# Optimization experiments

Measured on AMD Instinct MI355X. Metric: run time of the kernel, lower is better.

The kernel has to match this reference:

```python
import jax, jax.numpy as jnp
import numpy as np

PUPIL = 256          # pupil / OPD grid size
OUTPUT_DIM = 64      # cropped PSF postage-stamp size
N_BINS = 8           # number of SED wavelength bins
BATCH = 16
# Static, wavelength-dependent diffraction padding sizes (phase_N per bin).
# In the original these come from packed_SED_data[:,0,:] but are constant in a FoV.
PHASE_NS = [1024, 988, 952, 918, 886, 856, 828, 802]


def setup_inputs() -> dict:
    key = jax.random.key(0)
    k1, k2, k3 = jax.random.split(key, 3)
    # OPD in meters: small wavefront errors (~lambda/10 rms)
    opd_batch = jax.random.normal(k1, (BATCH, PUPIL, PUPIL), dtype=jnp.float32) * 1e-7
    # Annular pupil: outer aperture with central obscuration (like Euclid/VIS optics)
    yy, xx = np.mgrid[:PUPIL, :PUPIL].astype(np.float32)
    c = (PUPIL - 1) / 2.0
    r = np.sqrt((xx - c) ** 2 + (yy - c) ** 2) / (PUPIL / 2.0)
    obscurations = jnp.asarray(((r <= 1.0) & (r >= 0.3)).astype(np.float32))
    # Observed wavelengths per bin, in meters (visible band)
    lambdas = jnp.linspace(0.55e-6, 0.9e-6, N_BINS).astype(jnp.float32)
    # Normalized SED weights
    sed = jax.random.uniform(k2, (N_BINS,), dtype=jnp.float32) + 0.1
    sed_norms = sed / jnp.sum(sed)
    return {
        "opd_batch": opd_batch,
        "obscurations": obscurations,
        "lambdas": lambdas,
        "sed_norms": sed_norms,
    }


def _mono_psf(opd, obsc, lam, phase_N, out_dim):
    """Batched monochromatic PSF: OPD -> phase -> padded FFT -> cropped |.|^2, unit-sum."""
    # opd: [B, p, p]; phase = exp(i * 2pi/lambda * opd) * obscurations
    pre_phase = (2.0 * jnp.pi / lam) * opd
    phase = (jnp.cos(pre_phase) + 1j * jnp.sin(pre_phase)).astype(jnp.complex64)
    phase = phase * obsc.astype(jnp.complex64)
    p = opd.shape[-1]
    pad_lo = (phase_N - p) // 2
    pad_hi = phase_N - p - pad_lo
    padded = jnp.pad(phase, ((0, 0), (pad_lo, pad_hi), (pad_lo, pad_hi)))  # [B, N, N]
    fft = jnp.fft.fftshift(jnp.fft.fft2(padded), axes=(-2, -1))
    psf = fft.real ** 2 + fft.imag ** 2  # |FFT|^2, float32
    start = phase_N // 2 - out_dim // 2
    psf = psf[:, start:start + out_dim, start:start + out_dim]  # central crop
    return psf / jnp.sum(psf, axis=(-2, -1), keepdims=True)


def reference(opd_batch, obscurations, lambdas, sed_norms):
    # Polychromatic PSF: SED-weighted sum of monochromatic PSFs over wavelength bins.
    # Loop is over the small fixed set of bins (distinct static FFT sizes);
    # each bin is fully vectorized over the batch.
    out = jnp.zeros((opd_batch.shape[0], OUTPUT_DIM, OUTPUT_DIM), dtype=jnp.float32)
    for b, phase_N in enumerate(PHASE_NS):
        out = out + sed_norms[b] * _mono_psf(
            opd_batch, obscurations, lambdas[b], phase_N, OUTPUT_DIM
        )
    return out
```

## Files before the change

kernel.cpp:

```cpp
#include <hip/hip_runtime.h>
#include <math.h>

#define PUPIL 256
#define N_BINS 8
#define BATCH 16

__constant__ int PHASE_NS_C[N_BINS] = {1024, 988, 952, 918, 886, 856, 828, 802};

typedef short bf16x8 __attribute__((ext_vector_type(8)));
typedef float f32x4  __attribute__((ext_vector_type(4)));
typedef int   i32x4  __attribute__((ext_vector_type(4)));

#define MFMA16(a, b, c) __builtin_amdgcn_mfma_f32_16x16x32_bf16((a), (b), (c), 0, 0, 0)

__device__ __forceinline__ short f2bf(float f) {
  unsigned u = __float_as_uint(f);
  u += 0x7FFFu + ((u >> 16) & 1u);
  return (short)(u >> 16);
}
__device__ __forceinline__ bf16x8 neg8(bf16x8 v) {
  i32x4 t = __builtin_bit_cast(i32x4, v);
  t ^= (int)0x80008000;
  return __builtin_bit_cast(bf16x8, t);
}


__global__ void wprep(short* __restrict__ Wr_t, short* __restrict__ Wi_t) {
  int idx = blockIdx.x * 256 + threadIdx.x;
  int n   = idx & 255;
  int k   = (idx >> 8) & 63;
  int bin = idx >> 14;
  int N = PHASE_NS_C[bin];
  int m = ((k - 32) * n) % N;
  if (m < 0) m += N;
  float ang = -6.283185307179586f * (float)m / (float)N;
  float s, c;
  sincosf(ang, &s, &c);
  Wr_t[idx] = f2bf(c);
  Wi_t[idx] = f2bf(s);
}

__global__ __launch_bounds__(256, 1) void fused(
    const float* __restrict__ opd, const float* __restrict__ obsc,
    const float* __restrict__ lambdas,
    const short* __restrict__ Wr_t, const short* __restrict__ Wi_t,
    float* __restrict__ psf_raw, float* __restrict__ sums)
{
  const int tid = threadIdx.x;
  const int khalf = blockIdx.x, bin = blockIdx.y, b = blockIdx.z;
  const int bb = b * N_BINS + bin;
  const float w0 = 6.283185307179586f / lambdas[bin];

  __shared__ short Pr[256 * 40], Pi[256 * 40];
  __shared__ short Gr[32 * 264], Gi[32 * 264];
  __shared__ float pvbuf[64 * 33];
  __shared__ float red[4];

  const int wave = tid >> 6, lane = tid & 63;
  const int lr = lane & 15, lq = lane >> 4;

  f32x4 aR[2][4], aI[2][4];
  #pragma unroll
  for (int m = 0; m < 2; ++m)
    #pragma unroll
    for (int t = 0; t < 4; ++t) { aR[m][t] = (f32x4)0.0f; aI[m][t] = (f32x4)0.0f; }

  const int gy0 = tid >> 2;
  const int gx  = (tid & 3) * 8;
  const short* wr0 = Wr_t + ((size_t)bin * 64 + khalf * 32 + lr) * 256 + lq * 8;
  const short* wi0 = Wi_t + ((size_t)bin * 64 + khalf * 32 + lr) * 256 + lq * 8;

  for (int xc = 0; xc < 8; ++xc) {
    const int xb = xc * 32;
    bf16x8 vr[4], vi[4];
    #pragma unroll
    for (int i = 0; i < 4; ++i) {
      const int y = gy0 + i * 64;
      const float* orow = opd + ((size_t)b * PUPIL + y) * PUPIL + xb + gx;
      const float* brow = obsc + (size_t)y * PUPIL + xb + gx;
      float od[8], ob[8];
      *(float4*)&od[0] = *(const float4*)orow;
      *(float4*)&od[4] = *(const float4*)(orow + 4);
      *(float4*)&ob[0] = *(const float4*)brow;
      *(float4*)&ob[4] = *(const float4*)(brow + 4);
      #pragma unroll
      for (int j = 0; j < 8; ++j) {
        float s, c;
        __sincosf(w0 * od[j], &s, &c);
        vr[i][j] = f2bf(c * ob[j]);
        vi[i][j] = f2bf(s * ob[j]);
      }
    }
    __syncthreads();
    #pragma unroll
    for (int i = 0; i < 4; ++i) {
      const int y = gy0 + i * 64;
      *(bf16x8*)&Pr[y * 40 + gx] = vr[i];
      *(bf16x8*)&Pi[y * 40 + gx] = vi[i];
    }
    const bf16x8 w_r0  = *(const bf16x8*)(wr0 + xb);
    const bf16x8 w_r1  = *(const bf16x8*)(wr0 + 16 * 256 + xb);
    const bf16x8 w_i0  = *(const bf16x8*)(wi0 + xb);
    const bf16x8 w_i1  = *(const bf16x8*)(wi0 + 16 * 256 + xb);
    const bf16x8 nw_i0 = neg8(w_i0);
    const bf16x8 nw_i1 = neg8(w_i1);
    __syncthreads();

    for (int t = 0; t < 4; ++t) {
      const int y = wave * 64 + t * 16 + lr;
      const bf16x8 pr = *(const bf16x8*)&Pr[y * 40 + lq * 8];
      const bf16x8 pi = *(const bf16x8*)&Pi[y * 40 + lq * 8];
      aR[0][t] = MFMA16(w_r0,  pr, aR[0][t]);
      aR[0][t] = MFMA16(nw_i0, pi, aR[0][t]);
      aI[0][t] = MFMA16(w_r0,  pi, aI[0][t]);
      aI[0][t] = MFMA16(w_i0,  pr, aI[0][t]);
      aR[1][t] = MFMA16(w_r1,  pr, aR[1][t]);
      aR[1][t] = MFMA16(nw_i1, pi, aR[1][t]);
      aI[1][t] = MFMA16(w_r1,  pi, aI[1][t]);
      aI[1][t] = MFMA16(w_i1,  pr, aI[1][t]);
    }
  }

  #pragma unroll
  for (int m = 0; m < 2; ++m)
    #pragma unroll
    for (int t = 0; t < 4; ++t) {
      const int y = wave * 64 + t * 16 + lr;
      #pragma unroll
      for (int r = 0; r < 4; ++r) {
        const int kvl = m * 16 + lq * 4 + r;
        Gr[kvl * 264 + y] = f2bf(aR[m][t][r]);
        Gi[kvl * 264 + y] = f2bf(aI[m][t][r]);
      }
    }
  __syncthreads();

  f32x4 hR[2], hI[2];
  hR[0] = (f32x4)0.0f; hR[1] = (f32x4)0.0f;
  hI[0] = (f32x4)0.0f; hI[1] = (f32x4)0.0f;

  for (int yc = 0; yc < 8; ++yc) {
    const int yb2 = yc * 32;
    const size_t wo = ((size_t)bin * 64 + wave * 16 + lr) * 256 + yb2 + lq * 8;
    const bf16x8 w_r = *(const bf16x8*)(Wr_t + wo);
    const bf16x8 w_i = *(const bf16x8*)(Wi_t + wo);
    #pragma unroll
    for (int m = 0; m < 2; ++m) {
      const bf16x8 g_r = *(const bf16x8*)&Gr[(m * 16 + lr) * 264 + yb2 + lq * 8];
      const bf16x8 g_i = *(const bf16x8*)&Gi[(m * 16 + lr) * 264 + yb2 + lq * 8];
      const bf16x8 ng_i = neg8(g_i);
      hR[m] = MFMA16(g_r,  w_r, hR[m]);
      hR[m] = MFMA16(ng_i, w_i, hR[m]);
      hI[m] = MFMA16(g_r,  w_i, hI[m]);
      hI[m] = MFMA16(g_i,  w_r, hI[m]);
    }
  }

  float pv[2][4];
  float lsum = 0.f;
  #pragma unroll
  for (int m = 0; m < 2; ++m)
    #pragma unroll
    for (int r = 0; r < 4; ++r) {
      pv[m][r] = hR[m][r] * hR[m][r] + hI[m][r] * hI[m][r];
      lsum += pv[m][r];
    }
  #pragma unroll
  for (int off = 32; off > 0; off >>= 1) lsum += __shfl_down(lsum, off);
  if (lane == 0) red[wave] = lsum;

  const int u = wave * 16 + lr;
  #pragma unroll
  for (int m = 0; m < 2; ++m)
    #pragma unroll
    for (int r = 0; r < 4; ++r)
      pvbuf[u * 33 + m * 16 + lq * 4 + r] = pv[m][r];
  __syncthreads();

  if (tid == 0)
    sums[bb * 2 + khalf] = red[0] + red[1] + red[2] + red[3];

  #pragma unroll
  for (int k2 = 0; k2 < 8; ++k2) {
    const int i = tid + k2 * 256;
    const int uu = i >> 5, vl = i & 31;
    psf_raw[(size_t)bb * 4096 + uu * 64 + khalf * 32 + vl] = pvbuf[uu * 33 + vl];
  }
}

__global__ void combine(const float* __restrict__ psf_raw,
                        const float* __restrict__ sums,
                        const float* __restrict__ sed,
                        float* __restrict__ out) {
  __shared__ float sc[N_BINS];
  const int blk = blockIdx.x;
  const int b = blk >> 4;
  const int px = (blk & 15) * 256 + threadIdx.x;
  if (threadIdx.x < N_BINS) {
    const int bb = b * N_BINS + threadIdx.x;
    sc[threadIdx.x] = sed[threadIdx.x] / (sums[bb * 2] + sums[bb * 2 + 1]);
  }
  __syncthreads();
  float acc = 0.f;
  #pragma unroll
  for (int bin = 0; bin < N_BINS; ++bin)
    acc += sc[bin] * psf_raw[(size_t)(b * N_BINS + bin) * 4096 + px];
  out[b * 4096 + px] = acc;
}

extern "C" void kernel_launch(void* const* d_in, const int* in_sizes, int n_in,
                              void* d_out, int out_size, void* d_ws, size_t ws_size,
                              hipStream_t stream) {
  const float* opd     = (const float*)d_in[0];
  const float* obsc    = (const float*)d_in[1];
  const float* lambdas = (const float*)d_in[2];
  const float* sed     = (const float*)d_in[3];
  float* out = (float*)d_out;

  short* Wr_t   = (short*)d_ws;
  short* Wi_t   = Wr_t + (size_t)N_BINS * 64 * 256;
  float* psf_raw = (float*)(Wi_t + (size_t)N_BINS * 64 * 256);
  float* sums    = psf_raw + (size_t)BATCH * N_BINS * 4096;

  wprep<<<512, 256, 0, stream>>>(Wr_t, Wi_t);
  fused<<<dim3(2, N_BINS, BATCH), 256, 0, stream>>>(opd, obsc, lambdas,
                                                    Wr_t, Wi_t, psf_raw, sums);
  combine<<<256, 256, 0, stream>>>(psf_raw, sums, sed, out);
}
```

Measured before the change: 84.18 us.

## Double block size to 512 threads and use fast twiddle computation

```diff
diff --git a/kernel.cpp b/kernel.cpp
--- a/kernel.cpp
+++ b/kernel.cpp
@@ -31,16 +31,15 @@
   int k   = (idx >> 8) & 63;
   int bin = idx >> 14;
   int N = PHASE_NS_C[bin];
-  int m = ((k - 32) * n) % N;
-  if (m < 0) m += N;
-  float ang = -6.283185307179586f * (float)m / (float)N;
+  float f = __fdividef((float)((k - 32) * n), (float)N);
+  float rev = f - floorf(f);
   float s, c;
-  sincosf(ang, &s, &c);
+  __sincosf(-6.283185307179586f * rev, &s, &c);
   Wr_t[idx] = f2bf(c);
   Wi_t[idx] = f2bf(s);
 }
 
-__global__ __launch_bounds__(256, 1) void fused(
+__global__ __launch_bounds__(512, 2) void fused(
     const float* __restrict__ opd, const float* __restrict__ obsc,
     const float* __restrict__ lambdas,
     const short* __restrict__ Wr_t, const short* __restrict__ Wi_t,
@@ -51,19 +50,22 @@
   const int bb = b * N_BINS + bin;
   const float w0 = 6.283185307179586f / lambdas[bin];
 
-  __shared__ short Pr[256 * 40], Pi[256 * 40];
-  __shared__ short Gr[32 * 264], Gi[32 * 264];
-  __shared__ float pvbuf[64 * 33];
-  __shared__ float red[4];
+  __shared__ __align__(16) char smem[20480 * 2 + 16896 * 2 + 32];
+  short* Pr    = (short*)smem;
+  short* Pi    = (short*)(smem + 20480);
+  short* Gr    = (short*)(smem + 40960);
+  short* Gi    = (short*)(smem + 57856);
+  float* red   = (float*)(smem + 74752);
+  float* pvbuf = (float*)smem;
 
   const int wave = tid >> 6, lane = tid & 63;
   const int lr = lane & 15, lq = lane >> 4;
 
-  f32x4 aR[2][4], aI[2][4];
+  f32x4 aR[2][2], aI[2][2];
   #pragma unroll
   for (int m = 0; m < 2; ++m)
     #pragma unroll
-    for (int t = 0; t < 4; ++t) { aR[m][t] = (f32x4)0.0f; aI[m][t] = (f32x4)0.0f; }
+    for (int t = 0; t < 2; ++t) { aR[m][t] = (f32x4)0.0f; aI[m][t] = (f32x4)0.0f; }
 
   const int gy0 = tid >> 2;
   const int gx  = (tid & 3) * 8;
@@ -72,10 +74,10 @@
 
   for (int xc = 0; xc < 8; ++xc) {
     const int xb = xc * 32;
-    bf16x8 vr[4], vi[4];
-    #pragma unroll
-    for (int i = 0; i < 4; ++i) {
-      const int y = gy0 + i * 64;
+    bf16x8 vr[2], vi[2];
+    #pragma unroll
+    for (int i = 0; i < 2; ++i) {
+      const int y = gy0 + i * 128;
       const float* orow = opd + ((size_t)b * PUPIL + y) * PUPIL + xb + gx;
       const float* brow = obsc + (size_t)y * PUPIL + xb + gx;
       float od[8], ob[8];
@@ -91,13 +93,6 @@
         vi[i][j] = f2bf(s * ob[j]);
       }
     }
-    __syncthreads();
-    #pragma unroll
-    for (int i = 0; i < 4; ++i) {
-      const int y = gy0 + i * 64;
-      *(bf16x8*)&Pr[y * 40 + gx] = vr[i];
-      *(bf16x8*)&Pi[y * 40 + gx] = vi[i];
-    }
     const bf16x8 w_r0  = *(const bf16x8*)(wr0 + xb);
     const bf16x8 w_r1  = *(const bf16x8*)(wr0 + 16 * 256 + xb);
     const bf16x8 w_i0  = *(const bf16x8*)(wi0 + xb);
@@ -105,9 +100,16 @@
     const bf16x8 nw_i0 = neg8(w_i0);
     const bf16x8 nw_i1 = neg8(w_i1);
     __syncthreads();
-
-    for (int t = 0; t < 4; ++t) {
-      const int y = wave * 64 + t * 16 + lr;
+    #pragma unroll
+    for (int i = 0; i < 2; ++i) {
+      const int y = gy0 + i * 128;
+      *(bf16x8*)&Pr[y * 40 + gx] = vr[i];
+      *(bf16x8*)&Pi[y * 40 + gx] = vi[i];
+    }
+    __syncthreads();
+
+    for (int t = 0; t < 2; ++t) {
+      const int y = wave * 32 + t * 16 + lr;
       const bf16x8 pr = *(const bf16x8*)&Pr[y * 40 + lq * 8];
       const bf16x8 pi = *(const bf16x8*)&Pi[y * 40 + lq * 8];
       aR[0][t] = MFMA16(w_r0,  pr, aR[0][t]);
@@ -124,8 +126,8 @@
   #pragma unroll
   for (int m = 0; m < 2; ++m)
     #pragma unroll
-    for (int t = 0; t < 4; ++t) {
-      const int y = wave * 64 + t * 16 + lr;
+    for (int t = 0; t < 2; ++t) {
+      const int y = wave * 32 + t * 16 + lr;
       #pragma unroll
       for (int r = 0; r < 4; ++r) {
         const int kvl = m * 16 + lq * 4 + r;
@@ -135,54 +137,48 @@
     }
   __syncthreads();
 
-  f32x4 hR[2], hI[2];
-  hR[0] = (f32x4)0.0f; hR[1] = (f32x4)0.0f;
-  hI[0] = (f32x4)0.0f; hI[1] = (f32x4)0.0f;
+  const int m2  = wave >> 2;
+  const int kut = wave & 3;
+  f32x4 hR = (f32x4)0.0f, hI = (f32x4)0.0f;
 
   for (int yc = 0; yc < 8; ++yc) {
     const int yb2 = yc * 32;
-    const size_t wo = ((size_t)bin * 64 + wave * 16 + lr) * 256 + yb2 + lq * 8;
+    const size_t wo = ((size_t)bin * 64 + kut * 16 + lr) * 256 + yb2 + lq * 8;
     const bf16x8 w_r = *(const bf16x8*)(Wr_t + wo);
     const bf16x8 w_i = *(const bf16x8*)(Wi_t + wo);
-    #pragma unroll
-    for (int m = 0; m < 2; ++m) {
-      const bf16x8 g_r = *(const bf16x8*)&Gr[(m * 16 + lr) * 264 + yb2 + lq * 8];
-      const bf16x8 g_i = *(const bf16x8*)&Gi[(m * 16 + lr) * 264 + yb2 + lq * 8];
-      const bf16x8 ng_i = neg8(g_i);
-      hR[m] = MFMA16(g_r,  w_r, hR[m]);
-      hR[m] = MFMA16(ng_i, w_i, hR[m]);
-      hI[m] = MFMA16(g_r,  w_i, hI[m]);
-      hI[m] = MFMA16(g_i,  w_r, hI[m]);
-    }
-  }
-
-  float pv[2][4];
+    const bf16x8 g_r = *(const bf16x8*)&Gr[(m2 * 16 + lr) * 264 + yb2 + lq * 8];
+    const bf16x8 g_i = *(const bf16x8*)&Gi[(m2 * 16 + lr) * 264 + yb2 + lq * 8];
+    const bf16x8 ng_i = neg8(g_i);
+    hR = MFMA16(g_r,  w_r, hR);
+    hR = MFMA16(ng_i, w_i, hR);
+    hI = MFMA16(g_r,  w_i, hI);
+    hI = MFMA16(g_i,  w_r, hI);
+  }
+
+  float pv[4];
   float lsum = 0.f;
   #pragma unroll
-  for (int m = 0; m < 2; ++m)
-    #pragma unroll
-    for (int r = 0; r < 4; ++r) {
-      pv[m][r] = hR[m][r] * hR[m][r] + hI[m][r] * hI[m][r];
-      lsum += pv[m][r];
-    }
+  for (int r = 0; r < 4; ++r) {
+    pv[r] = hR[r] * hR[r] + hI[r] * hI[r];
+    lsum += pv[r];
+  }
   #pragma unroll
   for (int off = 32; off > 0; off >>= 1) lsum += __shfl_down(lsum, off);
   if (lane == 0) red[wave] = lsum;
 
-  const int u = wave * 16 + lr;
-  #pragma unroll
-  for (int m = 0; m < 2; ++m)
-    #pragma unroll
-    for (int r = 0; r < 4; ++r)
-      pvbuf[u * 33 + m * 16 + lq * 4 + r] = pv[m][r];
+  const int u = kut * 16 + lr;
+  #pragma unroll
+  for (int r = 0; r < 4; ++r)
+    pvbuf[u * 33 + m2 * 16 + lq * 4 + r] = pv[r];
   __syncthreads();
 
   if (tid == 0)
-    sums[bb * 2 + khalf] = red[0] + red[1] + red[2] + red[3];
-
-  #pragma unroll
-  for (int k2 = 0; k2 < 8; ++k2) {
-    const int i = tid + k2 * 256;
+    sums[bb * 2 + khalf] = red[0] + red[1] + red[2] + red[3]
+                         + red[4] + red[5] + red[6] + red[7];
+
+  #pragma unroll
+  for (int k2 = 0; k2 < 4; ++k2) {
+    const int i = tid + k2 * 512;
     const int uu = i >> 5, vl = i & 31;
     psf_raw[(size_t)bb * 4096 + uu * 64 + khalf * 32 + vl] = pvbuf[uu * 33 + vl];
   }
@@ -223,7 +219,7 @@
   float* sums    = psf_raw + (size_t)BATCH * N_BINS * 4096;
 
   wprep<<<512, 256, 0, stream>>>(Wr_t, Wi_t);
-  fused<<<dim3(2, N_BINS, BATCH), 256, 0, stream>>>(opd, obsc, lambdas,
+  fused<<<dim3(2, N_BINS, BATCH), 512, 0, stream>>>(opd, obsc, lambdas,
                                                     Wr_t, Wi_t, psf_raw, sums);
   combine<<<256, 256, 0, stream>>>(psf_raw, sums, sed, out);
 }
```

After: 86.72 us. +3.0%, slower.
